# Kernel optimization log

Measured on AMD Instinct MI355X. Metric: run time of the kernel, lower is better.

## Reference

```python
import jax, jax.numpy as jnp
import numpy as np

GROUP_SIZE = 128
QMIN, QMAX = -128.0, 127.0  # int8
EPS = 1.1920928955078125e-07  # float32 eps, guards zero scale


def setup_inputs() -> dict:
    key = jax.random.key(0)
    x = jax.random.normal(key, (8192, 8192), dtype=jnp.float32)
    return {"x": x}


def reference(x):
    # Dynamic per-group min/max observer + asymmetric int8 fake quantize.
    n, k = x.shape
    xg = x.reshape(n, k // GROUP_SIZE, GROUP_SIZE)  # [n, n_groups, g]
    # Observer: min/max per group, always including zero (asymmetric affine)
    mn = jnp.minimum(jnp.min(xg, axis=-1, keepdims=True), 0.0)
    mx = jnp.maximum(jnp.max(xg, axis=-1, keepdims=True), 0.0)
    scale = jnp.maximum((mx - mn) / (QMAX - QMIN), EPS)
    zero_point = jnp.clip(jnp.round(QMIN - mn / scale), QMIN, QMAX)  # int32 zp as float
    # scaled_fake_quantize: quantize -> clamp -> dequantize (round half-even)
    q = jnp.clip(jnp.round(xg / scale) + zero_point, QMIN, QMAX)
    return ((q - zero_point) * scale).reshape(n, k)
```

## Files before the change

kernel.cpp:

```cpp
#include <hip/hip_runtime.h>


typedef float f32x4 __attribute__((ext_vector_type(4)));

constexpr float QMIN = -128.0f;
constexpr float QMAX = 127.0f;
constexpr float EPSF = 1.1920928955078125e-07f;

__global__ __launch_bounds__(256) void dsq_kernel(
    const float* __restrict__ x, float* __restrict__ out, int n8) {
  const f32x4* __restrict__ x4 = reinterpret_cast<const f32x4*>(x);
  f32x4* __restrict__ o4 = reinterpret_cast<f32x4*>(out);

  int t = blockIdx.x * blockDim.x + threadIdx.x;
  int nthreads = gridDim.x * blockDim.x;

  for (int p = t; p < n8; p += nthreads) {
    int i0 = ((p >> 4) << 5) + (p & 15);
    f32x4 v0 = __builtin_nontemporal_load(&x4[i0]);
    f32x4 v1 = __builtin_nontemporal_load(&x4[i0 + 16]);

    float mn = fminf(fminf(fminf(v0.x, v0.y), fminf(v0.z, v0.w)),
                     fminf(fminf(v1.x, v1.y), fminf(v1.z, v1.w)));
    float mx = fmaxf(fmaxf(fmaxf(v0.x, v0.y), fmaxf(v0.z, v0.w)),
                     fmaxf(fmaxf(v1.x, v1.y), fmaxf(v1.z, v1.w)));

    #pragma unroll
    for (int m = 1; m < 16; m <<= 1) {
      mn = fminf(mn, __shfl_xor(mn, m, 64));
      mx = fmaxf(mx, __shfl_xor(mx, m, 64));
    }

    mn = fminf(mn, 0.0f);
    mx = fmaxf(mx, 0.0f);

    float scale = fmaxf((mx - mn) * (1.0f / 255.0f), EPSF);
    float inv = 1.0f / scale;
    float zp = fminf(fmaxf(rintf(QMIN - mn / scale), QMIN), QMAX);

    f32x4 o0, o1;
    o0.x = (fminf(fmaxf(rintf(v0.x * inv) + zp, QMIN), QMAX) - zp) * scale;
    o0.y = (fminf(fmaxf(rintf(v0.y * inv) + zp, QMIN), QMAX) - zp) * scale;
    o0.z = (fminf(fmaxf(rintf(v0.z * inv) + zp, QMIN), QMAX) - zp) * scale;
    o0.w = (fminf(fmaxf(rintf(v0.w * inv) + zp, QMIN), QMAX) - zp) * scale;
    o1.x = (fminf(fmaxf(rintf(v1.x * inv) + zp, QMIN), QMAX) - zp) * scale;
    o1.y = (fminf(fmaxf(rintf(v1.y * inv) + zp, QMIN), QMAX) - zp) * scale;
    o1.z = (fminf(fmaxf(rintf(v1.z * inv) + zp, QMIN), QMAX) - zp) * scale;
    o1.w = (fminf(fmaxf(rintf(v1.w * inv) + zp, QMIN), QMAX) - zp) * scale;

    __builtin_nontemporal_store(o0, &o4[i0]);
    __builtin_nontemporal_store(o1, &o4[i0 + 16]);
  }
}

extern "C" void kernel_launch(void* const* d_in, const int* in_sizes, int n_in,
                              void* d_out, int out_size, void* d_ws, size_t ws_size,
                              hipStream_t stream) {
  const float* x = (const float*)d_in[0];
  float* out = (float*)d_out;
  int n8 = out_size / 8;

  dsq_kernel<<<2048, 256, 0, stream>>>(x, out, n8);
}
```

Baseline: 418.1 us.

## Process 16 elements per thread with 8-lane groups and FMA dequantize

```diff
diff --git a/kernel.cpp b/kernel.cpp
--- a/kernel.cpp
+++ b/kernel.cpp
@@ -7,26 +7,33 @@
 constexpr float QMAX = 127.0f;
 constexpr float EPSF = 1.1920928955078125e-07f;
 
+__device__ __forceinline__ float min4(f32x4 v) {
+  return fminf(fminf(v.x, v.y), fminf(v.z, v.w));
+}
+__device__ __forceinline__ float max4(f32x4 v) {
+  return fmaxf(fmaxf(v.x, v.y), fmaxf(v.z, v.w));
+}
+
 __global__ __launch_bounds__(256) void dsq_kernel(
-    const float* __restrict__ x, float* __restrict__ out, int n8) {
+    const float* __restrict__ x, float* __restrict__ out, int n16) {
   const f32x4* __restrict__ x4 = reinterpret_cast<const f32x4*>(x);
   f32x4* __restrict__ o4 = reinterpret_cast<f32x4*>(out);
 
   int t = blockIdx.x * blockDim.x + threadIdx.x;
   int nthreads = gridDim.x * blockDim.x;
 
-  for (int p = t; p < n8; p += nthreads) {
-    int i0 = ((p >> 4) << 5) + (p & 15);
-    f32x4 v0 = __builtin_nontemporal_load(&x4[i0]);
-    f32x4 v1 = __builtin_nontemporal_load(&x4[i0 + 16]);
+  for (int p = t; p < n16; p += nthreads) {
+    int base = ((p >> 3) << 5) + (p & 7);
+    f32x4 v0 = x4[base];
+    f32x4 v1 = x4[base + 8];
+    f32x4 v2 = x4[base + 16];
+    f32x4 v3 = x4[base + 24];
 
-    float mn = fminf(fminf(fminf(v0.x, v0.y), fminf(v0.z, v0.w)),
-                     fminf(fminf(v1.x, v1.y), fminf(v1.z, v1.w)));
-    float mx = fmaxf(fmaxf(fmaxf(v0.x, v0.y), fmaxf(v0.z, v0.w)),
-                     fmaxf(fmaxf(v1.x, v1.y), fmaxf(v1.z, v1.w)));
+    float mn = fminf(fminf(min4(v0), min4(v1)), fminf(min4(v2), min4(v3)));
+    float mx = fmaxf(fmaxf(max4(v0), max4(v1)), fmaxf(max4(v2), max4(v3)));
 
     #pragma unroll
-    for (int m = 1; m < 16; m <<= 1) {
+    for (int m = 1; m < 8; m <<= 1) {
       mn = fminf(mn, __shfl_xor(mn, m, 64));
       mx = fmaxf(mx, __shfl_xor(mx, m, 64));
     }
@@ -37,19 +44,20 @@
     float scale = fmaxf((mx - mn) * (1.0f / 255.0f), EPSF);
     float inv = 1.0f / scale;
     float zp = fminf(fmaxf(rintf(QMIN - mn / scale), QMIN), QMAX);
+    float nzs = -zp * scale;
 
-    f32x4 o0, o1;
-    o0.x = (fminf(fmaxf(rintf(v0.x * inv) + zp, QMIN), QMAX) - zp) * scale;
-    o0.y = (fminf(fmaxf(rintf(v0.y * inv) + zp, QMIN), QMAX) - zp) * scale;
-    o0.z = (fminf(fmaxf(rintf(v0.z * inv) + zp, QMIN), QMAX) - zp) * scale;
-    o0.w = (fminf(fmaxf(rintf(v0.w * inv) + zp, QMIN), QMAX) - zp) * scale;
-    o1.x = (fminf(fmaxf(rintf(v1.x * inv) + zp, QMIN), QMAX) - zp) * scale;
-    o1.y = (fminf(fmaxf(rintf(v1.y * inv) + zp, QMIN), QMAX) - zp) * scale;
-    o1.z = (fminf(fmaxf(rintf(v1.z * inv) + zp, QMIN), QMAX) - zp) * scale;
-    o1.w = (fminf(fmaxf(rintf(v1.w * inv) + zp, QMIN), QMAX) - zp) * scale;
+    f32x4 o0, o1, o2, o3;
+    #define QDQ(e) fmaf(fminf(fmaxf(rintf((e) * inv) + zp, QMIN), QMAX), scale, nzs)
+    o0.x = QDQ(v0.x); o0.y = QDQ(v0.y); o0.z = QDQ(v0.z); o0.w = QDQ(v0.w);
+    o1.x = QDQ(v1.x); o1.y = QDQ(v1.y); o1.z = QDQ(v1.z); o1.w = QDQ(v1.w);
+    o2.x = QDQ(v2.x); o2.y = QDQ(v2.y); o2.z = QDQ(v2.z); o2.w = QDQ(v2.w);
+    o3.x = QDQ(v3.x); o3.y = QDQ(v3.y); o3.z = QDQ(v3.z); o3.w = QDQ(v3.w);
+    #undef QDQ
 
-    __builtin_nontemporal_store(o0, &o4[i0]);
-    __builtin_nontemporal_store(o1, &o4[i0 + 16]);
+    __builtin_nontemporal_store(o0, &o4[base]);
+    __builtin_nontemporal_store(o1, &o4[base + 8]);
+    __builtin_nontemporal_store(o2, &o4[base + 16]);
+    __builtin_nontemporal_store(o3, &o4[base + 24]);
   }
 }
 
@@ -58,7 +66,7 @@
                               hipStream_t stream) {
   const float* x = (const float*)d_in[0];
   float* out = (float*)d_out;
-  int n8 = out_size / 8;
+  int n16 = out_size / 16;
 
-  dsq_kernel<<<2048, 256, 0, stream>>>(x, out, n8);
+  dsq_kernel<<<2048, 256, 0, stream>>>(x, out, n16);
 }
```

Result: slower. 440.5 us (+5.4%).

## Split fused quantize into observer and apply kernels with per-group param buffer

Applied to the files above, without the earlier changes.

```diff
diff --git a/kernel.cpp b/kernel.cpp
--- a/kernel.cpp
+++ b/kernel.cpp
@@ -7,23 +7,27 @@
 constexpr float QMAX = 127.0f;
 constexpr float EPSF = 1.1920928955078125e-07f;
 
-__global__ __launch_bounds__(256) void dsq_kernel(
-    const float* __restrict__ x, float* __restrict__ out, int n8) {
+__device__ __forceinline__ float min4(f32x4 v) {
+  return fminf(fminf(v.x, v.y), fminf(v.z, v.w));
+}
+__device__ __forceinline__ float max4(f32x4 v) {
+  return fmaxf(fmaxf(v.x, v.y), fmaxf(v.z, v.w));
+}
+
+__global__ __launch_bounds__(256) void dsq_obs(
+    const float* __restrict__ x, f32x4* __restrict__ params, int n8) {
   const f32x4* __restrict__ x4 = reinterpret_cast<const f32x4*>(x);
-  f32x4* __restrict__ o4 = reinterpret_cast<f32x4*>(out);
 
   int t = blockIdx.x * blockDim.x + threadIdx.x;
   int nthreads = gridDim.x * blockDim.x;
 
   for (int p = t; p < n8; p += nthreads) {
     int i0 = ((p >> 4) << 5) + (p & 15);
-    f32x4 v0 = __builtin_nontemporal_load(&x4[i0]);
-    f32x4 v1 = __builtin_nontemporal_load(&x4[i0 + 16]);
+    f32x4 v0 = x4[i0];
+    f32x4 v1 = x4[i0 + 16];
 
-    float mn = fminf(fminf(fminf(v0.x, v0.y), fminf(v0.z, v0.w)),
-                     fminf(fminf(v1.x, v1.y), fminf(v1.z, v1.w)));
-    float mx = fmaxf(fmaxf(fmaxf(v0.x, v0.y), fmaxf(v0.z, v0.w)),
-                     fmaxf(fmaxf(v1.x, v1.y), fmaxf(v1.z, v1.w)));
+    float mn = fminf(min4(v0), min4(v1));
+    float mx = fmaxf(max4(v0), max4(v1));
 
     #pragma unroll
     for (int m = 1; m < 16; m <<= 1) {
@@ -31,25 +35,41 @@
       mx = fmaxf(mx, __shfl_xor(mx, m, 64));
     }
 
-    mn = fminf(mn, 0.0f);
-    mx = fmaxf(mx, 0.0f);
+    if ((p & 15) == 0) {
+      mn = fminf(mn, 0.0f);
+      mx = fmaxf(mx, 0.0f);
+      float scale = fmaxf((mx - mn) * (1.0f / 255.0f), EPSF);
+      float inv = 1.0f / scale;
+      float zp = fminf(fmaxf(rintf(QMIN - mn / scale), QMIN), QMAX);
+      f32x4 pr;
+      pr.x = scale; pr.y = inv; pr.z = zp; pr.w = -zp * scale;
+      params[p >> 4] = pr;
+    }
+  }
+}
 
-    float scale = fmaxf((mx - mn) * (1.0f / 255.0f), EPSF);
-    float inv = 1.0f / scale;
-    float zp = fminf(fmaxf(rintf(QMIN - mn / scale), QMIN), QMAX);
+__global__ __launch_bounds__(256) void dsq_apply(
+    const float* __restrict__ x, const f32x4* __restrict__ params,
+    float* __restrict__ out, int n4) {
+  const f32x4* __restrict__ x4 = reinterpret_cast<const f32x4*>(x);
+  f32x4* __restrict__ o4 = reinterpret_cast<f32x4*>(out);
 
-    f32x4 o0, o1;
-    o0.x = (fminf(fmaxf(rintf(v0.x * inv) + zp, QMIN), QMAX) - zp) * scale;
-    o0.y = (fminf(fmaxf(rintf(v0.y * inv) + zp, QMIN), QMAX) - zp) * scale;
-    o0.z = (fminf(fmaxf(rintf(v0.z * inv) + zp, QMIN), QMAX) - zp) * scale;
-    o0.w = (fminf(fmaxf(rintf(v0.w * inv) + zp, QMIN), QMAX) - zp) * scale;
-    o1.x = (fminf(fmaxf(rintf(v1.x * inv) + zp, QMIN), QMAX) - zp) * scale;
-    o1.y = (fminf(fmaxf(rintf(v1.y * inv) + zp, QMIN), QMAX) - zp) * scale;
-    o1.z = (fminf(fmaxf(rintf(v1.z * inv) + zp, QMIN), QMAX) - zp) * scale;
-    o1.w = (fminf(fmaxf(rintf(v1.w * inv) + zp, QMIN), QMAX) - zp) * scale;
+  int t = blockIdx.x * blockDim.x + threadIdx.x;
+  int nthreads = gridDim.x * blockDim.x;
 
-    __builtin_nontemporal_store(o0, &o4[i0]);
-    __builtin_nontemporal_store(o1, &o4[i0 + 16]);
+  #pragma unroll 2
+  for (int i = t; i < n4; i += nthreads) {
+    f32x4 v = x4[i];
+    f32x4 pr = params[i >> 5];
+    float scale = pr.x, inv = pr.y, zp = pr.z, nzs = pr.w;
+
+    f32x4 o;
+    o.x = fmaf(fminf(fmaxf(rintf(v.x * inv) + zp, QMIN), QMAX), scale, nzs);
+    o.y = fmaf(fminf(fmaxf(rintf(v.y * inv) + zp, QMIN), QMAX), scale, nzs);
+    o.z = fmaf(fminf(fmaxf(rintf(v.z * inv) + zp, QMIN), QMAX), scale, nzs);
+    o.w = fmaf(fminf(fmaxf(rintf(v.w * inv) + zp, QMIN), QMAX), scale, nzs);
+
+    __builtin_nontemporal_store(o, &o4[i]);
   }
 }
 
@@ -58,7 +78,11 @@
                               hipStream_t stream) {
   const float* x = (const float*)d_in[0];
   float* out = (float*)d_out;
+  f32x4* params = (f32x4*)d_ws;
+
   int n8 = out_size / 8;
+  int n4 = out_size / 4;
 
-  dsq_kernel<<<2048, 256, 0, stream>>>(x, out, n8);
+  dsq_obs<<<2048, 256, 0, stream>>>(x, params, n8);
+  dsq_apply<<<2048, 256, 0, stream>>>(x, params, out, n4);
 }
```

New measurement: 487.3 us. 16.5% more time.
